# Performance work log

Measured on AMD Instinct MI355X. Metric: run time of the kernel, lower is better.

## Reference

```python
import jax, jax.numpy as jnp
import numpy as np

B, D, H, L, T = 4096, 1024, 2048, 256, 8
STD = 0.02


def setup_inputs() -> dict:
    key = jax.random.key(0)
    ks = jax.random.split(key, 24)
    n = lambda k, shp: (jax.random.normal(k, shp, dtype=jnp.float32) * STD)
    inp = {
        "x": jax.random.uniform(ks[0], (B, D), dtype=jnp.float32),
        "task": jax.random.randint(ks[1], (B,), 0, T),
        "eps": jax.random.normal(ks[2], (B, L), dtype=jnp.float32),
        # per-task encoder stacks: in->H->H->H->2L
        "enc_W1": n(ks[3], (T, D, H)), "enc_b1": jnp.zeros((T, H)),
        "enc_W2": n(ks[4], (T, H, H)), "enc_b2": jnp.zeros((T, H)),
        "enc_W3": n(ks[5], (T, H, H)), "enc_b3": jnp.zeros((T, H)),
        "enc_W4": n(ks[6], (T, H, 2 * L)), "enc_b4": jnp.zeros((T, 2 * L)),
        # shared decoder (BayesianLinear means): L->H->H
        "ds_W1": n(ks[7], (L, H)), "ds_b1": jnp.zeros((H,)),
        "ds_W2": n(ks[8], (H, H)), "ds_b2": jnp.zeros((H,)),
        # per-task decoder heads: H->H->D with Sigmoid
        "hd_W1": n(ks[9], (T, H, H)), "hd_b1": jnp.zeros((T, H)),
        "hd_W2": n(ks[10], (T, H, D)), "hd_b2": jnp.zeros((T, D)),
    }
    return inp


def reference(x, task, eps,
              enc_W1, enc_b1, enc_W2, enc_b2, enc_W3, enc_b3, enc_W4, enc_b4,
              ds_W1, ds_b1, ds_W2, ds_b2,
              hd_W1, hd_b1, hd_W2, hd_b2):
    ntasks = enc_W1.shape[0]
    onehot = jax.nn.one_hot(task, ntasks, dtype=x.dtype)  # [B, T], the task==idx mask

    # ---- encode: run every task's encoder on the full batch, mask-sum ----
    def enc_one(W1, b1, W2, b2, W3, b3, W4, b4):
        h = jax.nn.relu(x @ W1 + b1)
        h = jax.nn.relu(h @ W2 + b2)
        h = jax.nn.relu(h @ W3 + b3)
        return h @ W4 + b4  # [B, 2L]

    enc_all = jax.vmap(enc_one)(enc_W1, enc_b1, enc_W2, enc_b2,
                                enc_W3, enc_b3, enc_W4, enc_b4)  # [T, B, 2L]
    scat = jnp.einsum('tbd,bt->bd', enc_all, onehot)  # [B, 2L]
    latent = scat.shape[1] // 2
    mu, log_sigma = scat[:, :latent], scat[:, latent:]
    z = mu + jnp.exp(log_sigma) * eps  # reparameterization

    # ---- decode: shared trunk, then every head masked ----
    h = jax.nn.relu(z @ ds_W1 + ds_b1)
    h = jax.nn.relu(h @ ds_W2 + ds_b2)  # [B, H]

    def head_one(W1, b1, W2, b2):
        g = jax.nn.relu(h @ W1 + b1)
        return jax.nn.sigmoid(g @ W2 + b2)  # [B, D]

    heads_all = jax.vmap(head_one)(hd_W1, hd_b1, hd_W2, hd_b2)  # [T, B, D]
    return jnp.einsum('tbd,bt->bd', heads_all, onehot)  # [B, D]
```

## Files before the change

### kernel.cpp

```cpp
#include <hip/hip_runtime.h>
#include <hip/hip_bf16.h>

#define T_TASKS 8
#define B_ROWS 4096
#define PADROWS 4224
#define BM 128
#define BN 64
#define BK 32
#define MAXTILES 40

typedef __attribute__((ext_vector_type(4))) float f32x4;
typedef __attribute__((ext_vector_type(8))) short bf16x8;

#define GLOAD_LDS16(g, l) __builtin_amdgcn_global_load_lds( \
    (const __attribute__((address_space(1))) void*)(g), \
    (__attribute__((address_space(3))) void*)(l), 16, 0, 0)

__device__ __forceinline__ unsigned short f32_to_bf16(float f) {
    union { float f; unsigned int u; } v; v.f = f;
    unsigned int r = v.u + 0x7FFF + ((v.u >> 16) & 1);
    return (unsigned short)(r >> 16);
}

__device__ __forceinline__ unsigned int pack2_bf16(float lo, float hi) {
    __hip_bfloat162 h = __float22bfloat162_rn(make_float2(lo, hi));
    union { __hip_bfloat162 h; unsigned int u; } c; c.h = h;
    return c.u;
}

__global__ void setup_kernel(const int* __restrict__ task, int* __restrict__ perm,
                             int* __restrict__ offs, int* __restrict__ table) {
    __shared__ int cnt[T_TASKS];
    __shared__ int cur[T_TASKS];
    int tid = threadIdx.x;
    if (tid < T_TASKS) cnt[tid] = 0;
    __syncthreads();
    for (int b = tid; b < B_ROWS; b += blockDim.x)
        atomicAdd(&cnt[task[b]], 1);
    __syncthreads();
    if (tid == 0) {
        int o = 0;
        for (int t = 0; t < T_TASKS; ++t) { offs[t] = o; cur[t] = o; o += cnt[t]; }
        offs[T_TASKS] = o;
        int s = 0;
        for (int t = 0; t < T_TASKS; ++t) {
            int nt = (cnt[t] + BM - 1) / BM;
            for (int j = 0; j < nt; ++j) table[s++] = (t << 16) | j;
        }
        for (; s < MAXTILES; ++s) table[s] = -1;
    }
    __syncthreads();
    for (int b = tid; b < B_ROWS; b += blockDim.x) {
        int t = task[b];
        int pos = atomicAdd(&cur[t], 1);
        perm[pos] = b;
    }
}

__global__ void permute_cast_kernel(const float* __restrict__ x, const int* __restrict__ perm,
                                    unsigned short* __restrict__ xp) {
    int rowp = blockIdx.x;
    int src = perm[rowp];
    const float4* xin = reinterpret_cast<const float4*>(x + (size_t)src * 1024);
    unsigned short* dst = xp + (size_t)rowp * 1024;
    int c4 = threadIdx.x;
    float4 v = xin[c4];
    ushort4 o;
    o.x = f32_to_bf16(v.x); o.y = f32_to_bf16(v.y);
    o.z = f32_to_bf16(v.z); o.w = f32_to_bf16(v.w);
    *reinterpret_cast<ushort4*>(dst + c4 * 4) = o;
}

__global__ void vae_kernel(const float* __restrict__ scat, const float* __restrict__ eps,
                           const int* __restrict__ perm, unsigned short* __restrict__ z) {
    int rowp = blockIdx.x;
    int c = threadIdx.x;
    int src = perm[rowp];
    float mu = scat[(size_t)rowp * 512 + c];
    float ls = scat[(size_t)rowp * 512 + 256 + c];
    float e  = eps[(size_t)src * 256 + c];
    z[(size_t)rowp * 256 + c] = f32_to_bf16(mu + __expf(ls) * e);
}

template<int MODE>
__global__ __launch_bounds__(256, 6)
void gemm10_kernel(const unsigned short* __restrict__ A,
                   const float* __restrict__ W,
                   const float* __restrict__ bias, void* __restrict__ dst,
                   const int* __restrict__ offs, const int* __restrict__ table,
                   const int* __restrict__ perm,
                   int K, int N, int ldd, int Btot, int GX)
{
    __shared__ unsigned short As[2][BM * BK];
    __shared__ unsigned short Bs[2][BN * BK];

    const int bxh = blockIdx.x;
    const int tid = threadIdx.x;

    int bx = (bxh & 7) * (GX >> 3) + (bxh >> 3);

    int t, mtile, off, cnt;
    if (table != nullptr) {
        int v = table[bx];
        if (v < 0) return;
        t = v >> 16; mtile = v & 0xFFFF;
        off = offs[t]; cnt = offs[t + 1] - off;
    } else {
        t = 0; mtile = bx; off = 0; cnt = Btot;
    }
    const int n0 = blockIdx.y * BN;

    const int lane = tid & 63;
    const int wave = tid >> 6;
    const int wr = wave >> 1, wc = wave & 1;

    const int rl   = lane >> 2;
    const int csrc = ((lane & 3) ^ ((rl >> 1) & 3)) * 8;
    const unsigned short* Ab = A + ((size_t)(off + mtile * BM + rl)) * K + csrc;

    const int bn = lane;
    const int bc = wave;
    const float* Wb = W + (size_t)t * K * N + n0 + bn;
    const int bslot = (bc ^ ((bn >> 1) & 3)) * 8;
    float br[8];

    auto stage_a = [&](int buf, int k0) {
        #pragma unroll
        for (int jj = 0; jj < 2; ++jj) {
            int j = wave * 2 + jj;
            GLOAD_LDS16(Ab + (size_t)(j * 16) * K + k0, &As[buf][j * 512]);
        }
    };
    auto load_b = [&](int k0) {
        const float* p = Wb + (size_t)(k0 + bc * 8) * N;
        #pragma unroll
        for (int j = 0; j < 8; ++j)
            br[j] = p[(size_t)j * N];
    };
    auto write_b = [&](int buf) {
        uint4 wv;
        wv.x = pack2_bf16(br[0], br[1]);
        wv.y = pack2_bf16(br[2], br[3]);
        wv.z = pack2_bf16(br[4], br[5]);
        wv.w = pack2_bf16(br[6], br[7]);
        *reinterpret_cast<uint4*>(&Bs[buf][bn * 32 + bslot]) = wv;
    };

    f32x4 acc[4][2];
    #pragma unroll
    for (int m = 0; m < 4; ++m)
        #pragma unroll
        for (int n = 0; n < 2; ++n)
            acc[m][n] = (f32x4){0.f, 0.f, 0.f, 0.f};

    auto compute = [&](int buf) {
        bf16x8 af[4], bfr[2];
        #pragma unroll
        for (int m = 0; m < 4; ++m) {
            int rf = wr * 64 + m * 16 + (lane & 15);
            af[m] = *reinterpret_cast<const bf16x8*>(
                &As[buf][rf * 32 + (((lane >> 4) ^ ((rf >> 1) & 3)) * 8)]);
        }
        #pragma unroll
        for (int n = 0; n < 2; ++n) {
            int nf = wc * 32 + n * 16 + (lane & 15);
            bfr[n] = *reinterpret_cast<const bf16x8*>(
                &Bs[buf][nf * 32 + (((lane >> 4) ^ ((nf >> 1) & 3)) * 8)]);
        }
        #pragma unroll
        for (int m = 0; m < 4; ++m)
            #pragma unroll
            for (int n = 0; n < 2; ++n)
                acc[m][n] = __builtin_amdgcn_mfma_f32_16x16x32_bf16(af[m], bfr[n], acc[m][n], 0, 0, 0);
    };

    const int nsteps = K / BK;
    load_b(0);
    stage_a(0, 0);
    write_b(0);
    __syncthreads();

    int cur = 0;
    for (int s = 0; s < nsteps; ++s) {
        if (s + 1 < nsteps) {
            load_b((s + 1) * BK);
            stage_a(cur ^ 1, (s + 1) * BK);
        }
        compute(cur);
        if (s + 1 < nsteps) write_b(cur ^ 1);
        __syncthreads();
        cur ^= 1;
    }

    const float* bt = bias + (size_t)t * N;
    #pragma unroll
    for (int n = 0; n < 2; ++n) {
        int col = n0 + wc * 32 + n * 16 + (lane & 15);
        float bv = bt[col];
        #pragma unroll
        for (int m = 0; m < 4; ++m) {
            int rbase = mtile * BM + wr * 64 + m * 16 + ((lane >> 4) << 2);
            #pragma unroll
            for (int j = 0; j < 4; ++j) {
                int local = rbase + j;
                if (local >= cnt) continue;
                float v = acc[m][n][j] + bv;
                if (MODE == 0) {
                    ((unsigned short*)dst)[(size_t)(off + local) * ldd + col] =
                        f32_to_bf16(fmaxf(v, 0.f));
                } else if (MODE == 1) {
                    ((float*)dst)[(size_t)(off + local) * ldd + col] = v;
                } else {
                    int grow = perm[off + local];
                    ((float*)dst)[(size_t)grow * ldd + col] = 1.f / (1.f + __expf(-v));
                }
            }
        }
    }
}

extern "C" void kernel_launch(void* const* d_in, const int* in_sizes, int n_in,
                              void* d_out, int out_size, void* d_ws, size_t ws_size,
                              hipStream_t stream) {
    const float* x      = (const float*)d_in[0];
    const int*   task   = (const int*)d_in[1];
    const float* eps    = (const float*)d_in[2];
    const float* enc_W1 = (const float*)d_in[3];
    const float* enc_b1 = (const float*)d_in[4];
    const float* enc_W2 = (const float*)d_in[5];
    const float* enc_b2 = (const float*)d_in[6];
    const float* enc_W3 = (const float*)d_in[7];
    const float* enc_b3 = (const float*)d_in[8];
    const float* enc_W4 = (const float*)d_in[9];
    const float* enc_b4 = (const float*)d_in[10];
    const float* ds_W1  = (const float*)d_in[11];
    const float* ds_b1  = (const float*)d_in[12];
    const float* ds_W2  = (const float*)d_in[13];
    const float* ds_b2  = (const float*)d_in[14];
    const float* hd_W1  = (const float*)d_in[15];
    const float* hd_b1  = (const float*)d_in[16];
    const float* hd_W2  = (const float*)d_in[17];
    const float* hd_b2  = (const float*)d_in[18];
    float* out = (float*)d_out;

    char* ws = (char*)d_ws;
    int* perm  = (int*)ws;
    int* offs  = (int*)(ws + 16384);
    int* table = (int*)(ws + 16384 + 256);
    char* p = ws + 32768;
    unsigned short* xp = (unsigned short*)p; p += (size_t)PADROWS * 1024 * 2;
    unsigned short* h1 = (unsigned short*)p; p += (size_t)PADROWS * 2048 * 2;
    unsigned short* h2 = (unsigned short*)p; p += (size_t)PADROWS * 2048 * 2;
    unsigned short* zb = (unsigned short*)p; p += (size_t)PADROWS * 256 * 2;
    float* scat = out;

    setup_kernel<<<1, 1024, 0, stream>>>(task, perm, offs, table);
    permute_cast_kernel<<<B_ROWS, 256, 0, stream>>>(x, perm, xp);

    gemm10_kernel<0><<<dim3(MAXTILES, 32), 256, 0, stream>>>(xp, enc_W1, enc_b1, h1, offs, table, nullptr, 1024, 2048, 2048, B_ROWS, MAXTILES);
    gemm10_kernel<0><<<dim3(MAXTILES, 32), 256, 0, stream>>>(h1, enc_W2, enc_b2, h2, offs, table, nullptr, 2048, 2048, 2048, B_ROWS, MAXTILES);
    gemm10_kernel<0><<<dim3(MAXTILES, 32), 256, 0, stream>>>(h2, enc_W3, enc_b3, h1, offs, table, nullptr, 2048, 2048, 2048, B_ROWS, MAXTILES);
    gemm10_kernel<1><<<dim3(MAXTILES, 8), 256, 0, stream>>>(h1, enc_W4, enc_b4, scat, offs, table, nullptr, 2048, 512, 512, B_ROWS, MAXTILES);

    vae_kernel<<<B_ROWS, 256, 0, stream>>>(scat, eps, perm, zb);

    gemm10_kernel<0><<<dim3(32, 32), 256, 0, stream>>>(zb, ds_W1, ds_b1, h2, nullptr, nullptr, nullptr, 256, 2048, 2048, B_ROWS, 32);
    gemm10_kernel<0><<<dim3(32, 32), 256, 0, stream>>>(h2, ds_W2, ds_b2, h1, nullptr, nullptr, nullptr, 2048, 2048, 2048, B_ROWS, 32);

    gemm10_kernel<0><<<dim3(MAXTILES, 32), 256, 0, stream>>>(h1, hd_W1, hd_b1, h2, offs, table, nullptr, 2048, 2048, 2048, B_ROWS, MAXTILES);
    gemm10_kernel<2><<<dim3(MAXTILES, 16), 256, 0, stream>>>(h2, hd_W2, hd_b2, out, offs, table, perm, 2048, 1024, 1024, B_ROWS, MAXTILES);
}
```

Measured before the change: 670.4 us.

## Enlarge GEMM tiles to 256x256 with 512-thread blocks

Replaces the 128x64 GEMM tile with a 256x256 tile computed by 8 waves, each owning a 64x128 sub-block, and updates the task tile table and launch grids to match. Each fp32 weight tile is now converted to bf16 and reused across more rows, and each activation tile across more columns, so global traffic per FLOP drops. The cost is far fewer blocks per launch (e.g. 192 for the 2048-wide layers), which may leave many CUs idle. It also raises register use (128 accumulator floats per thread) and doubles shared memory per block.

```diff
diff --git a/kernel.cpp b/kernel.cpp
--- a/kernel.cpp
+++ b/kernel.cpp
@@ -3,11 +3,11 @@
 
 #define T_TASKS 8
 #define B_ROWS 4096
-#define PADROWS 4224
-#define BM 128
-#define BN 64
+#define PADROWS 4352
+#define BM 256
+#define BN 256
 #define BK 32
-#define MAXTILES 40
+#define MAXT256 24
 
 typedef __attribute__((ext_vector_type(4))) float f32x4;
 typedef __attribute__((ext_vector_type(8))) short bf16x8;
@@ -47,7 +47,7 @@
             int nt = (cnt[t] + BM - 1) / BM;
             for (int j = 0; j < nt; ++j) table[s++] = (t << 16) | j;
         }
-        for (; s < MAXTILES; ++s) table[s] = -1;
+        for (; s < MAXT256; ++s) table[s] = -1;
     }
     __syncthreads();
     for (int b = tid; b < B_ROWS; b += blockDim.x) {
@@ -83,13 +83,13 @@
 }
 
 template<int MODE>
-__global__ __launch_bounds__(256, 6)
-void gemm10_kernel(const unsigned short* __restrict__ A,
-                   const float* __restrict__ W,
-                   const float* __restrict__ bias, void* __restrict__ dst,
-                   const int* __restrict__ offs, const int* __restrict__ table,
-                   const int* __restrict__ perm,
-                   int K, int N, int ldd, int Btot, int GX)
+__global__ __launch_bounds__(512, 2)
+void gemm256_kernel(const unsigned short* __restrict__ A,
+                    const float* __restrict__ W,
+                    const float* __restrict__ bias, void* __restrict__ dst,
+                    const int* __restrict__ offs, const int* __restrict__ table,
+                    const int* __restrict__ perm,
+                    int K, int N, int ldd, int Btot, int GX)
 {
     __shared__ unsigned short As[2][BM * BK];
     __shared__ unsigned short Bs[2][BN * BK];
@@ -112,17 +112,18 @@
 
     const int lane = tid & 63;
     const int wave = tid >> 6;
-    const int wr = wave >> 1, wc = wave & 1;
+    const int wr = wave >> 1;
+    const int wc = wave & 1;
 
     const int rl   = lane >> 2;
     const int csrc = ((lane & 3) ^ ((rl >> 1) & 3)) * 8;
     const unsigned short* Ab = A + ((size_t)(off + mtile * BM + rl)) * K + csrc;
 
-    const int bn = lane;
-    const int bc = wave;
+    const int bn = tid & 255;
+    const int bc = tid >> 8;
     const float* Wb = W + (size_t)t * K * N + n0 + bn;
-    const int bslot = (bc ^ ((bn >> 1) & 3)) * 8;
-    float br[8];
+    const int swz = (bn >> 1) & 3;
+    float br[16];
 
     auto stage_a = [&](int buf, int k0) {
         #pragma unroll
@@ -132,10 +133,10 @@
         }
     };
     auto load_b = [&](int k0) {
-        const float* p = Wb + (size_t)(k0 + bc * 8) * N;
-        #pragma unroll
-        for (int j = 0; j < 8; ++j)
-            br[j] = p[(size_t)j * N];
+        const float* p = Wb + (size_t)(k0 + bc * 16) * N;
+        #pragma unroll
+        for (int r = 0; r < 16; ++r)
+            br[r] = p[(size_t)r * N];
     };
     auto write_b = [&](int buf) {
         uint4 wv;
@@ -143,18 +144,23 @@
         wv.y = pack2_bf16(br[2], br[3]);
         wv.z = pack2_bf16(br[4], br[5]);
         wv.w = pack2_bf16(br[6], br[7]);
-        *reinterpret_cast<uint4*>(&Bs[buf][bn * 32 + bslot]) = wv;
-    };
-
-    f32x4 acc[4][2];
+        *reinterpret_cast<uint4*>(&Bs[buf][bn * 32 + (((bc * 2) ^ swz) * 8)]) = wv;
+        wv.x = pack2_bf16(br[8], br[9]);
+        wv.y = pack2_bf16(br[10], br[11]);
+        wv.z = pack2_bf16(br[12], br[13]);
+        wv.w = pack2_bf16(br[14], br[15]);
+        *reinterpret_cast<uint4*>(&Bs[buf][bn * 32 + (((bc * 2 + 1) ^ swz) * 8)]) = wv;
+    };
+
+    f32x4 acc[4][8];
     #pragma unroll
     for (int m = 0; m < 4; ++m)
         #pragma unroll
-        for (int n = 0; n < 2; ++n)
+        for (int n = 0; n < 8; ++n)
             acc[m][n] = (f32x4){0.f, 0.f, 0.f, 0.f};
 
     auto compute = [&](int buf) {
-        bf16x8 af[4], bfr[2];
+        bf16x8 af[4], bfr[8];
         #pragma unroll
         for (int m = 0; m < 4; ++m) {
             int rf = wr * 64 + m * 16 + (lane & 15);
@@ -162,15 +168,15 @@
                 &As[buf][rf * 32 + (((lane >> 4) ^ ((rf >> 1) & 3)) * 8)]);
         }
         #pragma unroll
-        for (int n = 0; n < 2; ++n) {
-            int nf = wc * 32 + n * 16 + (lane & 15);
+        for (int n = 0; n < 8; ++n) {
+            int nf = wc * 128 + n * 16 + (lane & 15);
             bfr[n] = *reinterpret_cast<const bf16x8*>(
                 &Bs[buf][nf * 32 + (((lane >> 4) ^ ((nf >> 1) & 3)) * 8)]);
         }
         #pragma unroll
         for (int m = 0; m < 4; ++m)
             #pragma unroll
-            for (int n = 0; n < 2; ++n)
+            for (int n = 0; n < 8; ++n)
                 acc[m][n] = __builtin_amdgcn_mfma_f32_16x16x32_bf16(af[m], bfr[n], acc[m][n], 0, 0, 0);
     };
 
@@ -194,8 +200,8 @@
 
     const float* bt = bias + (size_t)t * N;
     #pragma unroll
-    for (int n = 0; n < 2; ++n) {
-        int col = n0 + wc * 32 + n * 16 + (lane & 15);
+    for (int n = 0; n < 8; ++n) {
+        int col = n0 + wc * 128 + n * 16 + (lane & 15);
         float bv = bt[col];
         #pragma unroll
         for (int m = 0; m < 4; ++m) {
@@ -257,16 +263,16 @@
     setup_kernel<<<1, 1024, 0, stream>>>(task, perm, offs, table);
     permute_cast_kernel<<<B_ROWS, 256, 0, stream>>>(x, perm, xp);
 
-    gemm10_kernel<0><<<dim3(MAXTILES, 32), 256, 0, stream>>>(xp, enc_W1, enc_b1, h1, offs, table, nullptr, 1024, 2048, 2048, B_ROWS, MAXTILES);
-    gemm10_kernel<0><<<dim3(MAXTILES, 32), 256, 0, stream>>>(h1, enc_W2, enc_b2, h2, offs, table, nullptr, 2048, 2048, 2048, B_ROWS, MAXTILES);
-    gemm10_kernel<0><<<dim3(MAXTILES, 32), 256, 0, stream>>>(h2, enc_W3, enc_b3, h1, offs, table, nullptr, 2048, 2048, 2048, B_ROWS, MAXTILES);
-    gemm10_kernel<1><<<dim3(MAXTILES, 8), 256, 0, stream>>>(h1, enc_W4, enc_b4, scat, offs, table, nullptr, 2048, 512, 512, B_ROWS, MAXTILES);
+    gemm256_kernel<0><<<dim3(MAXT256, 8), 512, 0, stream>>>(xp, enc_W1, enc_b1, h1, offs, table, nullptr, 1024, 2048, 2048, B_ROWS, MAXT256);
+    gemm256_kernel<0><<<dim3(MAXT256, 8), 512, 0, stream>>>(h1, enc_W2, enc_b2, h2, offs, table, nullptr, 2048, 2048, 2048, B_ROWS, MAXT256);
+    gemm256_kernel<0><<<dim3(MAXT256, 8), 512, 0, stream>>>(h2, enc_W3, enc_b3, h1, offs, table, nullptr, 2048, 2048, 2048, B_ROWS, MAXT256);
+    gemm256_kernel<1><<<dim3(MAXT256, 2), 512, 0, stream>>>(h1, enc_W4, enc_b4, scat, offs, table, nullptr, 2048, 512, 512, B_ROWS, MAXT256);
 
     vae_kernel<<<B_ROWS, 256, 0, stream>>>(scat, eps, perm, zb);
 
-    gemm10_kernel<0><<<dim3(32, 32), 256, 0, stream>>>(zb, ds_W1, ds_b1, h2, nullptr, nullptr, nullptr, 256, 2048, 2048, B_ROWS, 32);
-    gemm10_kernel<0><<<dim3(32, 32), 256, 0, stream>>>(h2, ds_W2, ds_b2, h1, nullptr, nullptr, nullptr, 2048, 2048, 2048, B_ROWS, 32);
-
-    gemm10_kernel<0><<<dim3(MAXTILES, 32), 256, 0, stream>>>(h1, hd_W1, hd_b1, h2, offs, table, nullptr, 2048, 2048, 2048, B_ROWS, MAXTILES);
-    gemm10_kernel<2><<<dim3(MAXTILES, 16), 256, 0, stream>>>(h2, hd_W2, hd_b2, out, offs, table, perm, 2048, 1024, 1024, B_ROWS, MAXTILES);
-}
+    gemm256_kernel<0><<<dim3(16, 8), 512, 0, stream>>>(zb, ds_W1, ds_b1, h2, nullptr, nullptr, nullptr, 256, 2048, 2048, B_ROWS, 16);
+    gemm256_kernel<0><<<dim3(16, 8), 512, 0, stream>>>(h2, ds_W2, ds_b2, h1, nullptr, nullptr, nullptr, 2048, 2048, 2048, B_ROWS, 16);
+
+    gemm256_kernel<0><<<dim3(MAXT256, 8), 512, 0, stream>>>(h1, hd_W1, hd_b1, h2, offs, table, nullptr, 2048, 2048, 2048, B_ROWS, MAXT256);
+    gemm256_kernel<2><<<dim3(MAXT256, 4), 512, 0, stream>>>(h2, hd_W2, hd_b2, out, offs, table, perm, 2048, 1024, 1024, B_ROWS, MAXT256);
+}
```

Result: slower. 942.1 us (+40.5%).
